# Optimization experiments

Measured on AMD Instinct MI355X. Metric: run time of the kernel, lower is better.

Reference implementation:

```python
import jax, jax.numpy as jnp
import numpy as np

B, C, E, H = 8, 2048, 1024, 128


def setup_inputs() -> dict:
    key = jax.random.key(0)
    k1, k2, k3, k4 = jax.random.split(key, 4)
    x = jax.random.normal(k1, (B, C, E), dtype=jnp.float32)
    # store projection weights as (E, H) so projection is x @ W
    Wq = jax.random.normal(k2, (E, H), dtype=jnp.float32) * (E ** -0.5)
    Wk = jax.random.normal(k3, (E, H), dtype=jnp.float32) * (E ** -0.5)
    Wv = jax.random.normal(k4, (E, H), dtype=jnp.float32) * (E ** -0.5)
    return {"x": x, "Wq": Wq, "Wk": Wk, "Wv": Wv}


def reference(x, Wq, Wk, Wv):
    # x: (B, C, E) -> out: (B, C, H)
    _, c, e = x.shape
    q = x @ Wq  # (B, C, H)
    k = x @ Wk  # (B, C, H)
    v = x @ Wv  # (B, C, H)
    # NOTE: original scales by embed_size**0.5, not head_size**0.5
    scale = jnp.asarray(e, x.dtype) ** 0.5
    w = jnp.einsum('bqh,bkh->bqk', q, k) / scale  # (B, C, C)
    causal = jnp.tril(jnp.ones((c, c), dtype=bool))
    w = jnp.where(causal, w, -jnp.inf)
    w = jax.nn.softmax(w, axis=-1)
    # dropout_rate = 0.0 -> identity (eval mode)
    out = w @ v  # (B, C, H)
    return out
```

## Files before the change

kernel.cpp:

```cpp
#include <hip/hip_runtime.h>
#include <hip/hip_bf16.h>
#include <stdint.h>

#define B_ 8
#define C_ 2048
#define E_ 1024
#define H_ 128
#define M_ (B_*C_)
#define SLOTS_B 144

typedef __attribute__((ext_vector_type(8))) short bf16x8;
typedef __attribute__((ext_vector_type(4))) float f32x4;

__device__ __forceinline__ unsigned short f2bf(float f) {
    union { float f; unsigned int u; } v; v.f = f;
    unsigned int u = v.u;
    u += 0x7fff + ((u >> 16) & 1);
    return (unsigned short)(u >> 16);
}
__device__ __forceinline__ float bf2f(unsigned short u) {
    union { unsigned int i; float f; } v; v.i = ((unsigned int)u) << 16; return v.f;
}

#define GLOAD_LDS16(g, l) \
    __builtin_amdgcn_global_load_lds((const __attribute__((address_space(1))) void*)(g), \
                                     (__attribute__((address_space(3))) void*)(l), 16, 0, 0)

__global__ __launch_bounds__(256) void wt_kernel(const float* __restrict__ Wq,
                                                 const float* __restrict__ Wk,
                                                 const float* __restrict__ Wv,
                                                 unsigned short* __restrict__ WT) {
    int z = blockIdx.y;
    const float* W = (z == 0) ? Wq : (z == 1) ? Wk : Wv;
    unsigned short* o = WT + (size_t)z * H_ * E_;
    int idx = blockIdx.x * 256 + threadIdx.x;
    int e = idx & (E_ - 1), h = idx >> 10;
    o[(size_t)h * E_ + e] = f2bf(W[(size_t)e * H_ + h]);
}

__global__ __launch_bounds__(256) void proj_kernel(const float* __restrict__ x,
                                                   const unsigned short* __restrict__ WT,
                                                   unsigned short* __restrict__ QKV) {
    __shared__ __align__(16) unsigned short As[32][64];
    __shared__ __align__(16) unsigned short Bs[3][128][64];

    const int tid = threadIdx.x;
    const int wid = tid >> 6, lane = tid & 63;
    const int lrow = lane & 15, lq = lane >> 4;
    const int wc = wid;
    const int row0 = blockIdx.x * 32;

    const int arow = tid >> 3;
    const int ag = tid & 7;

    f32x4 acc[3][2][2];
#pragma unroll
    for (int w = 0; w < 3; ++w)
#pragma unroll
        for (int mi = 0; mi < 2; ++mi)
#pragma unroll
            for (int ni = 0; ni < 2; ++ni) acc[w][mi][ni] = (f32x4){0.f, 0.f, 0.f, 0.f};

    for (int k0 = 0; k0 < E_; k0 += 64) {
        const float* xs = x + (size_t)(row0 + arow) * E_ + k0 + ag * 8;
        float4 a0 = *(const float4*)xs;
        float4 a1 = *(const float4*)(xs + 4);
        __syncthreads();
        {
            unsigned short t0[8] = {f2bf(a0.x), f2bf(a0.y), f2bf(a0.z), f2bf(a0.w),
                                    f2bf(a1.x), f2bf(a1.y), f2bf(a1.z), f2bf(a1.w)};
            *(bf16x8*)&As[arow][(ag ^ (arow & 7)) * 8] = *(const bf16x8*)t0;
        }
#pragma unroll
        for (int w = 0; w < 3; ++w)
#pragma unroll
            for (int s = 0; s < 4; ++s) {
                int brow = s * 32 + (tid >> 3);
                int bg = (tid & 7) ^ (brow & 7);
                const unsigned short* src = WT + (size_t)w * H_ * E_ + (size_t)brow * E_ + k0 + bg * 8;
                char* dst = (char*)&Bs[w][0][0] + s * 4096 + tid * 16;
                GLOAD_LDS16(src, dst);
            }
        __syncthreads();
#pragma unroll
        for (int ks = 0; ks < 2; ++ks) {
            const int g = ks * 4 + lq;
            bf16x8 af[2];
#pragma unroll
            for (int mi = 0; mi < 2; ++mi) {
                int ra = mi * 16 + lrow;
                af[mi] = *(const bf16x8*)&As[ra][(g ^ (ra & 7)) * 8];
            }
#pragma unroll
            for (int w = 0; w < 3; ++w)
#pragma unroll
                for (int ni = 0; ni < 2; ++ni) {
                    int rb = wc * 32 + ni * 16 + lrow;
                    bf16x8 bb = *(const bf16x8*)&Bs[w][rb][(g ^ (rb & 7)) * 8];
#pragma unroll
                    for (int mi = 0; mi < 2; ++mi)
                        acc[w][mi][ni] = __builtin_amdgcn_mfma_f32_16x16x32_bf16(af[mi], bb, acc[w][mi][ni], 0, 0, 0);
                }
        }
    }

#pragma unroll
    for (int w = 0; w < 2; ++w) {
        const float qs = (w == 0) ? 0.03125f : 1.0f;
        unsigned short* outp = QKV + (size_t)w * M_ * H_;
#pragma unroll
        for (int mi = 0; mi < 2; ++mi) {
            int r0 = row0 + mi * 16 + lq * 4;
#pragma unroll
            for (int ni = 0; ni < 2; ++ni) {
                int col = wc * 32 + ni * 16 + lrow;
#pragma unroll
                for (int r = 0; r < 4; ++r)
                    outp[(size_t)(r0 + r) * H_ + col] = f2bf(acc[w][mi][ni][r] * qs);
            }
        }
    }
    {
        unsigned short* vt = QKV + (size_t)2 * M_ * H_;
        int b = row0 / C_;
        int cbase = row0 % C_;
#pragma unroll
        for (int mi = 0; mi < 2; ++mi) {
            int c0 = cbase + mi * 16 + lq * 4;
#pragma unroll
            for (int ni = 0; ni < 2; ++ni) {
                int h = wc * 32 + ni * 16 + lrow;
                __align__(8) unsigned short p[4] = {f2bf(acc[2][mi][ni][0]), f2bf(acc[2][mi][ni][1]),
                                                    f2bf(acc[2][mi][ni][2]), f2bf(acc[2][mi][ni][3])};
                *(uint2*)&vt[((size_t)b * H_ + h) * C_ + c0] = *(const uint2*)p;
            }
        }
    }
}

__global__ __launch_bounds__(256) void attn_kernel(const unsigned short* __restrict__ QKV,
                                                   unsigned short* __restrict__ PO,
                                                   float* __restrict__ ML,
                                                   float* __restrict__ out) {
    __shared__ __align__(16) unsigned short Ks[2][64][128];
    __shared__ __align__(16) unsigned short Vt[2][128][64];
    __shared__ __align__(16) unsigned short Ps[4][16][72];

    const unsigned short* Q  = QKV;
    const unsigned short* K  = QKV + (size_t)M_ * H_;
    const unsigned short* VT = QKV + (size_t)2 * M_ * H_;

    const int tid = threadIdx.x, wid = tid >> 6, lane = tid & 63;
    const int lrow = lane & 15, lq = lane >> 4, lk = lq * 8;
    const int rr = blockIdx.x;
    const int b = blockIdx.y;

    int j = 0;
#pragma unroll
    for (int jj = 1; jj < 32; ++jj) {
        int q = jj >> 2, s = jj & 3;
        if (jj + 2 * q * (q - 1) + s * q <= rr) j = jj;
    }
    const int qj = j >> 2, sj = j & 3;
    const int Cj = j + 2 * qj * (qj - 1) + sj * qj;
    const int c = rr - Cj;
    const int nch = qj + 1;
    const int t0 = c * 4;
    const int t1 = min(t0 + 4, j + 1);

    const int q0w = j * 64 + wid * 16;
    const unsigned short* Kb  = K  + (size_t)b * C_ * H_;
    const unsigned short* VTb = VT + (size_t)b * H_ * C_;
    const int qrow0 = q0w + lq * 4;

    const int krow = tid >> 4, kg = tid & 15;
    const int vrow = tid >> 3, vg = tid & 7;

    bf16x8 qf[4];
#pragma unroll
    for (int kf = 0; kf < 4; ++kf)
        qf[kf] = *(const bf16x8*)&Q[((size_t)b * C_ + q0w + lrow) * H_ + kf * 32 + lk];

    f32x4 o[8];
#pragma unroll
    for (int nf = 0; nf < 8; ++nf) o[nf] = (f32x4){0.f, 0.f, 0.f, 0.f};
    float m[4] = {-INFINITY, -INFINITY, -INFINITY, -INFINITY};
    float l[4] = {0.f, 0.f, 0.f, 0.f};

    auto STAGE = [&](int buf, int t) {
        const int kv0 = t * 64;
#pragma unroll
        for (int s = 0; s < 4; ++s) {
            int r = s * 16 + krow;
            GLOAD_LDS16(&Kb[(size_t)(kv0 + r) * H_ + ((kg ^ (r & 15)) * 8)],
                        (char*)&Ks[buf][0][0] + s * 4096 + tid * 16);
        }
#pragma unroll
        for (int s = 0; s < 4; ++s) {
            int h = s * 32 + vrow;
            GLOAD_LDS16(&VTb[(size_t)h * C_ + kv0 + ((vg ^ (h & 7)) * 8)],
                        (char*)&Vt[buf][0][0] + s * 4096 + tid * 16);
        }
    };

    STAGE(0, t0);

    for (int t = t0; t < t1; ++t) {
        const int cur = (t - t0) & 1;
        __syncthreads();
        if (t + 1 < t1) STAGE(cur ^ 1, t + 1);

        const int kv0 = t * 64;
        f32x4 s[4];
#pragma unroll
        for (int nf = 0; nf < 4; ++nf) {
            s[nf] = (f32x4){0.f, 0.f, 0.f, 0.f};
            const int rk = nf * 16 + lrow;
#pragma unroll
            for (int kf = 0; kf < 4; ++kf) {
                bf16x8 kb = *(const bf16x8*)&Ks[cur][rk][((kf * 4 + lq) ^ (rk & 15)) * 8];
                s[nf] = __builtin_amdgcn_mfma_f32_16x16x32_bf16(qf[kf], kb, s[nf], 0, 0, 0);
            }
        }
        bf16x8 vb[8][2];
#pragma unroll
        for (int nf = 0; nf < 8; ++nf) {
            const int h = nf * 16 + lrow;
#pragma unroll
            for (int kf2 = 0; kf2 < 2; ++kf2)
                vb[nf][kf2] = *(const bf16x8*)&Vt[cur][h][((kf2 * 4 + lq) ^ (h & 7)) * 8];
        }

        if (t == j) {
#pragma unroll
            for (int nf = 0; nf < 4; ++nf) {
                int key = kv0 + nf * 16 + lrow;
#pragma unroll
                for (int r = 0; r < 4; ++r)
                    if (key > qrow0 + r) s[nf][r] = -INFINITY;
            }
        }
        float mt[4] = {-INFINITY, -INFINITY, -INFINITY, -INFINITY};
#pragma unroll
        for (int nf = 0; nf < 4; ++nf)
#pragma unroll
            for (int r = 0; r < 4; ++r) mt[r] = fmaxf(mt[r], s[nf][r]);
#pragma unroll
        for (int r = 0; r < 4; ++r)
#pragma unroll
            for (int off = 1; off < 16; off <<= 1)
                mt[r] = fmaxf(mt[r], __shfl_xor(mt[r], off));

        float corr[4];
#pragma unroll
        for (int r = 0; r < 4; ++r) {
            float mn = fmaxf(m[r], mt[r]);
            corr[r] = __expf(m[r] - mn);
            m[r] = mn;
        }
        float ps[4] = {0.f, 0.f, 0.f, 0.f};
#pragma unroll
        for (int nf = 0; nf < 4; ++nf)
#pragma unroll
            for (int r = 0; r < 4; ++r) {
                float p = __expf(s[nf][r] - m[r]);
                ps[r] += p;
                Ps[wid][lq * 4 + r][nf * 16 + lrow] = f2bf(p);
            }
#pragma unroll
        for (int r = 0; r < 4; ++r) {
#pragma unroll
            for (int off = 1; off < 16; off <<= 1) ps[r] += __shfl_xor(ps[r], off);
            l[r] = l[r] * corr[r] + ps[r];
        }
#pragma unroll
        for (int nf = 0; nf < 8; ++nf)
#pragma unroll
            for (int r = 0; r < 4; ++r) o[nf][r] *= corr[r];

        bf16x8 pa[2];
#pragma unroll
        for (int kf2 = 0; kf2 < 2; ++kf2)
            pa[kf2] = *(const bf16x8*)&Ps[wid][lrow][kf2 * 32 + lk];
#pragma unroll
        for (int nf = 0; nf < 8; ++nf)
#pragma unroll
            for (int kf2 = 0; kf2 < 2; ++kf2)
                o[nf] = __builtin_amdgcn_mfma_f32_16x16x32_bf16(pa[kf2], vb[nf][kf2], o[nf], 0, 0, 0);
    }

    if (nch == 1) {
#pragma unroll
        for (int nf = 0; nf < 8; ++nf) {
            int col = nf * 16 + lrow;
#pragma unroll
            for (int r = 0; r < 4; ++r)
                out[((size_t)b * C_ + qrow0 + r) * H_ + col] = o[nf][r] / l[r];
        }
    } else {
        const int slot = b * SLOTS_B + rr;
        unsigned short* po = PO + (size_t)slot * 64 * 128;
        const int rl0 = wid * 16 + lq * 4;
#pragma unroll
        for (int nf = 0; nf < 8; ++nf) {
            int col = nf * 16 + lrow;
#pragma unroll
            for (int r = 0; r < 4; ++r)
                po[(size_t)(rl0 + r) * 128 + col] = f2bf(o[nf][r]);
        }
        if (lrow == 0) {
            float* ml = ML + (size_t)slot * 128;
#pragma unroll
            for (int r = 0; r < 4; ++r) {
                ml[rl0 + r] = m[r];
                ml[64 + rl0 + r] = l[r];
            }
        }
    }
}

__global__ __launch_bounds__(256) void combine_kernel(const unsigned short* __restrict__ PO,
                                                      const float* __restrict__ ML,
                                                      float* __restrict__ out) {
    const int j = blockIdx.x + 4;
    const int b = blockIdx.y;
    const int q = j >> 2, s = j & 3;
    const int Cj = j + 2 * q * (q - 1) + s * q;
    const int nch = q + 1;
    const int base = b * SLOTS_B + Cj;
    const int row = threadIdx.x >> 2;
    const int colg = (threadIdx.x & 3) * 32;

    float mstar = -INFINITY;
    for (int c = 0; c < nch; ++c)
        mstar = fmaxf(mstar, ML[(size_t)(base + c) * 128 + row]);

    float denom = 0.f;
    float acc[32];
#pragma unroll
    for (int i = 0; i < 32; ++i) acc[i] = 0.f;

    for (int c = 0; c < nch; ++c) {
        float mc = ML[(size_t)(base + c) * 128 + row];
        float lc = ML[(size_t)(base + c) * 128 + 64 + row];
        float w = __expf(mc - mstar);
        denom += w * lc;
        const unsigned short* p = PO + (size_t)(base + c) * 64 * 128 + (size_t)row * 128 + colg;
#pragma unroll
        for (int k = 0; k < 4; ++k) {
            bf16x8 v = *(const bf16x8*)&p[k * 8];
#pragma unroll
            for (int e = 0; e < 8; ++e)
                acc[k * 8 + e] += w * bf2f(((unsigned short*)&v)[e]);
        }
    }
    float inv = 1.f / denom;
    float* op = out + ((size_t)b * C_ + j * 64 + row) * H_ + colg;
#pragma unroll
    for (int k = 0; k < 8; ++k) {
        float4 st = {acc[k * 4] * inv, acc[k * 4 + 1] * inv, acc[k * 4 + 2] * inv, acc[k * 4 + 3] * inv};
        *(float4*)&op[k * 4] = st;
    }
}

extern "C" void kernel_launch(void* const* d_in, const int* in_sizes, int n_in,
                              void* d_out, int out_size, void* d_ws, size_t ws_size,
                              hipStream_t stream) {
    const float* x  = (const float*)d_in[0];
    const float* Wq = (const float*)d_in[1];
    const float* Wk = (const float*)d_in[2];
    const float* Wv = (const float*)d_in[3];
    float* out = (float*)d_out;

    unsigned short* WT  = (unsigned short*)d_ws;
    unsigned short* QKV = WT + (size_t)3 * H_ * E_;
    unsigned short* PO  = QKV + (size_t)3 * M_ * H_;
    float*          ML  = (float*)(PO + (size_t)8 * SLOTS_B * 64 * 128);

    wt_kernel<<<dim3(H_ * E_ / 256, 3), 256, 0, stream>>>(Wq, Wk, Wv, WT);
    proj_kernel<<<dim3(M_ / 32), 256, 0, stream>>>(x, WT, QKV);
    attn_kernel<<<dim3(SLOTS_B, B_), 256, 0, stream>>>(QKV, PO, ML, out);
    combine_kernel<<<dim3(28, B_), 256, 0, stream>>>(PO, ML, out);
}
```

Measured before the change: 81.39 us.

## Split projection grid per weight matrix and double-buffer LDS tiles

The projection kernel now launches one grid slice per weight (Q, K, V) with 64-row tiles and a 2x2 wave layout. It double-buffers the A and B tiles in LDS so the global loads for the next k-step overlap the MFMA work on the current one. The x tile is now read and converted three times, once per weight matrix, instead of once, which adds global traffic on the fp32 input. In exchange it gains more blocks, one barrier per iteration and better latency hiding.

```diff
diff --git a/kernel.cpp b/kernel.cpp
--- a/kernel.cpp
+++ b/kernel.cpp
@@ -41,97 +41,114 @@
 __global__ __launch_bounds__(256) void proj_kernel(const float* __restrict__ x,
                                                    const unsigned short* __restrict__ WT,
                                                    unsigned short* __restrict__ QKV) {
-    __shared__ __align__(16) unsigned short As[32][64];
-    __shared__ __align__(16) unsigned short Bs[3][128][64];
+    __shared__ __align__(16) unsigned short As[2][64][64];
+    __shared__ __align__(16) unsigned short Bs[2][128][64];
 
     const int tid = threadIdx.x;
     const int wid = tid >> 6, lane = tid & 63;
     const int lrow = lane & 15, lq = lane >> 4;
-    const int wc = wid;
-    const int row0 = blockIdx.x * 32;
-
-    const int arow = tid >> 3;
-    const int ag = tid & 7;
-
-    f32x4 acc[3][2][2];
-#pragma unroll
-    for (int w = 0; w < 3; ++w)
-#pragma unroll
-        for (int mi = 0; mi < 2; ++mi)
-#pragma unroll
-            for (int ni = 0; ni < 2; ++ni) acc[w][mi][ni] = (f32x4){0.f, 0.f, 0.f, 0.f};
-
-    for (int k0 = 0; k0 < E_; k0 += 64) {
-        const float* xs = x + (size_t)(row0 + arow) * E_ + k0 + ag * 8;
-        float4 a0 = *(const float4*)xs;
-        float4 a1 = *(const float4*)(xs + 4);
-        __syncthreads();
-        {
-            unsigned short t0[8] = {f2bf(a0.x), f2bf(a0.y), f2bf(a0.z), f2bf(a0.w),
-                                    f2bf(a1.x), f2bf(a1.y), f2bf(a1.z), f2bf(a1.w)};
-            *(bf16x8*)&As[arow][(ag ^ (arow & 7)) * 8] = *(const bf16x8*)t0;
-        }
-#pragma unroll
-        for (int w = 0; w < 3; ++w)
-#pragma unroll
-            for (int s = 0; s < 4; ++s) {
-                int brow = s * 32 + (tid >> 3);
-                int bg = (tid & 7) ^ (brow & 7);
-                const unsigned short* src = WT + (size_t)w * H_ * E_ + (size_t)brow * E_ + k0 + bg * 8;
-                char* dst = (char*)&Bs[w][0][0] + s * 4096 + tid * 16;
-                GLOAD_LDS16(src, dst);
-            }
-        __syncthreads();
+    const int wr = wid >> 1, wc = wid & 1;
+    const int row0 = blockIdx.x * 64;
+    const int w = blockIdx.y;
+    const unsigned short* wt = WT + (size_t)w * H_ * E_;
+
+    const int arow = tid >> 2;
+    const int ag0 = (tid & 3) * 2;
+    const float* xrow = x + (size_t)(row0 + arow) * E_ + ag0 * 8;
+
+    f32x4 acc[2][4];
+#pragma unroll
+    for (int mi = 0; mi < 2; ++mi)
+#pragma unroll
+        for (int ni = 0; ni < 4; ++ni) acc[mi][ni] = (f32x4){0.f, 0.f, 0.f, 0.f};
+
+    float4 a0, a1, a2, a3;
+    auto A_LOAD = [&](int t) {
+        const float* xs = xrow + t * 64;
+        a0 = *(const float4*)xs;       a1 = *(const float4*)(xs + 4);
+        a2 = *(const float4*)(xs + 8); a3 = *(const float4*)(xs + 12);
+    };
+    auto A_WRITE = [&](int buf) {
+        unsigned short t0[8] = {f2bf(a0.x), f2bf(a0.y), f2bf(a0.z), f2bf(a0.w),
+                                f2bf(a1.x), f2bf(a1.y), f2bf(a1.z), f2bf(a1.w)};
+        unsigned short t1[8] = {f2bf(a2.x), f2bf(a2.y), f2bf(a2.z), f2bf(a2.w),
+                                f2bf(a3.x), f2bf(a3.y), f2bf(a3.z), f2bf(a3.w)};
+        *(bf16x8*)&As[buf][arow][(ag0 ^ (arow & 7)) * 8]       = *(const bf16x8*)t0;
+        *(bf16x8*)&As[buf][arow][((ag0 + 1) ^ (arow & 7)) * 8] = *(const bf16x8*)t1;
+    };
+    auto B_STAGE = [&](int buf, int t) {
+#pragma unroll
+        for (int s = 0; s < 4; ++s) {
+            int brow = s * 32 + (tid >> 3);
+            int bg = (tid & 7) ^ (brow & 7);
+            GLOAD_LDS16(wt + (size_t)brow * E_ + t * 64 + bg * 8,
+                        (char*)&Bs[buf][0][0] + s * 4096 + tid * 16);
+        }
+    };
+    auto COMPUTE = [&](int buf) {
 #pragma unroll
         for (int ks = 0; ks < 2; ++ks) {
             const int g = ks * 4 + lq;
-            bf16x8 af[2];
+            bf16x8 af[2], bfr[4];
 #pragma unroll
             for (int mi = 0; mi < 2; ++mi) {
-                int ra = mi * 16 + lrow;
-                af[mi] = *(const bf16x8*)&As[ra][(g ^ (ra & 7)) * 8];
-            }
-#pragma unroll
-            for (int w = 0; w < 3; ++w)
-#pragma unroll
-                for (int ni = 0; ni < 2; ++ni) {
-                    int rb = wc * 32 + ni * 16 + lrow;
-                    bf16x8 bb = *(const bf16x8*)&Bs[w][rb][(g ^ (rb & 7)) * 8];
-#pragma unroll
-                    for (int mi = 0; mi < 2; ++mi)
-                        acc[w][mi][ni] = __builtin_amdgcn_mfma_f32_16x16x32_bf16(af[mi], bb, acc[w][mi][ni], 0, 0, 0);
-                }
-        }
-    }
-
-#pragma unroll
-    for (int w = 0; w < 2; ++w) {
+                int ra = wr * 32 + mi * 16 + lrow;
+                af[mi] = *(const bf16x8*)&As[buf][ra][(g ^ (ra & 7)) * 8];
+            }
+#pragma unroll
+            for (int ni = 0; ni < 4; ++ni) {
+                int rb = wc * 64 + ni * 16 + lrow;
+                bfr[ni] = *(const bf16x8*)&Bs[buf][rb][(g ^ (rb & 7)) * 8];
+            }
+#pragma unroll
+            for (int mi = 0; mi < 2; ++mi)
+#pragma unroll
+                for (int ni = 0; ni < 4; ++ni)
+                    acc[mi][ni] = __builtin_amdgcn_mfma_f32_16x16x32_bf16(af[mi], bfr[ni], acc[mi][ni], 0, 0, 0);
+        }
+    };
+
+    A_LOAD(0);
+    B_STAGE(0, 0);
+    A_WRITE(0);
+
+    for (int t = 0; t < 16; ++t) {
+        const int cur = t & 1;
+        __syncthreads();
+        if (t < 15) {
+            A_LOAD(t + 1);
+            B_STAGE(cur ^ 1, t + 1);
+        }
+        COMPUTE(cur);
+        if (t < 15) A_WRITE(cur ^ 1);
+    }
+
+    if (w < 2) {
         const float qs = (w == 0) ? 0.03125f : 1.0f;
         unsigned short* outp = QKV + (size_t)w * M_ * H_;
 #pragma unroll
         for (int mi = 0; mi < 2; ++mi) {
-            int r0 = row0 + mi * 16 + lq * 4;
-#pragma unroll
-            for (int ni = 0; ni < 2; ++ni) {
-                int col = wc * 32 + ni * 16 + lrow;
+            int r0 = row0 + wr * 32 + mi * 16 + lq * 4;
+#pragma unroll
+            for (int ni = 0; ni < 4; ++ni) {
+                int col = wc * 64 + ni * 16 + lrow;
 #pragma unroll
                 for (int r = 0; r < 4; ++r)
-                    outp[(size_t)(r0 + r) * H_ + col] = f2bf(acc[w][mi][ni][r] * qs);
-            }
-        }
-    }
-    {
+                    outp[(size_t)(r0 + r) * H_ + col] = f2bf(acc[mi][ni][r] * qs);
+            }
+        }
+    } else {
         unsigned short* vt = QKV + (size_t)2 * M_ * H_;
         int b = row0 / C_;
         int cbase = row0 % C_;
 #pragma unroll
         for (int mi = 0; mi < 2; ++mi) {
-            int c0 = cbase + mi * 16 + lq * 4;
-#pragma unroll
-            for (int ni = 0; ni < 2; ++ni) {
-                int h = wc * 32 + ni * 16 + lrow;
-                __align__(8) unsigned short p[4] = {f2bf(acc[2][mi][ni][0]), f2bf(acc[2][mi][ni][1]),
-                                                    f2bf(acc[2][mi][ni][2]), f2bf(acc[2][mi][ni][3])};
+            int c0 = cbase + wr * 32 + mi * 16 + lq * 4;
+#pragma unroll
+            for (int ni = 0; ni < 4; ++ni) {
+                int h = wc * 64 + ni * 16 + lrow;
+                __align__(8) unsigned short p[4] = {f2bf(acc[mi][ni][0]), f2bf(acc[mi][ni][1]),
+                                                    f2bf(acc[mi][ni][2]), f2bf(acc[mi][ni][3])};
                 *(uint2*)&vt[((size_t)b * H_ + h) * C_ + c0] = *(const uint2*)p;
             }
         }
@@ -378,7 +395,7 @@
     float*          ML  = (float*)(PO + (size_t)8 * SLOTS_B * 64 * 128);
 
     wt_kernel<<<dim3(H_ * E_ / 256, 3), 256, 0, stream>>>(Wq, Wk, Wv, WT);
-    proj_kernel<<<dim3(M_ / 32), 256, 0, stream>>>(x, WT, QKV);
+    proj_kernel<<<dim3(M_ / 64, 3), 256, 0, stream>>>(x, WT, QKV);
     attn_kernel<<<dim3(SLOTS_B, B_), 256, 0, stream>>>(QKV, PO, ML, out);
     combine_kernel<<<dim3(28, B_), 256, 0, stream>>>(PO, ML, out);
 }
```

Result: no change. 81.43 us (+0.1%).
